# Performance work log

Hardware: AMD Instinct MI355X
Metric: run time of the kernel (lower is better)

Reference implementation:

```python
import jax, jax.numpy as jnp
import numpy as np
from jax import lax

RES = 14
DIM = 384
KEY_DIM = 32
NUM_HEADS = 12
ATTN_RATIO = 4
NH_KD = KEY_DIM * NUM_HEADS            # 384
DH = ATTN_RATIO * KEY_DIM * NUM_HEADS  # 1536
HQKV = DH + 2 * NH_KD                  # 2304
BN_EPS = 1e-5


def _bias_idxs():
    ys, xs = np.meshgrid(np.arange(RES), np.arange(RES), indexing='ij')
    ys = ys.reshape(-1); xs = xs.reshape(-1)
    dy = np.abs(ys[:, None] - ys[None, :])
    dx = np.abs(xs[:, None] - xs[None, :])
    return jnp.asarray(dy * RES + dx, dtype=jnp.int32)  # [196,196], 196 unique offsets


def setup_inputs() -> dict:
    key = jax.random.key(0)
    ks = jax.random.split(key, 16)
    B = 128
    x = jax.random.normal(ks[0], (B, DIM, RES, RES), dtype=jnp.float32)
    # qkv: 1x1 conv DIM->HQKV + BN
    qkv_w = jax.random.normal(ks[1], (HQKV, DIM, 1, 1), dtype=jnp.float32) * 0.05
    qkv_g = jax.random.normal(ks[2], (HQKV,), dtype=jnp.float32) * 0.1 + 1.0
    qkv_b = jax.random.normal(ks[3], (HQKV,), dtype=jnp.float32) * 0.1
    qkv_m = jax.random.normal(ks[4], (HQKV,), dtype=jnp.float32) * 0.1
    qkv_v = jax.random.uniform(ks[5], (HQKV,), dtype=jnp.float32) + 0.5
    # dw: depthwise 3x3 conv on q channels + BN
    dw_w = jax.random.normal(ks[6], (NH_KD, 1, 3, 3), dtype=jnp.float32) * 0.2
    dw_g = jax.random.normal(ks[7], (NH_KD,), dtype=jnp.float32) * 0.1 + 1.0
    dw_b = jax.random.normal(ks[8], (NH_KD,), dtype=jnp.float32) * 0.1
    dw_m = jax.random.normal(ks[9], (NH_KD,), dtype=jnp.float32) * 0.1
    dw_v = jax.random.uniform(ks[10], (NH_KD,), dtype=jnp.float32) + 0.5
    # proj: ReLU -> 1x1 conv DH->DIM + BN
    proj_w = jax.random.normal(ks[11], (DIM, DH, 1, 1), dtype=jnp.float32) * 0.05
    proj_g = jax.random.normal(ks[12], (DIM,), dtype=jnp.float32) * 0.1 + 1.0
    proj_b = jax.random.normal(ks[13], (DIM,), dtype=jnp.float32) * 0.1
    proj_m = jax.random.normal(ks[14], (DIM,), dtype=jnp.float32) * 0.1
    proj_v = jax.random.uniform(ks[15], (DIM,), dtype=jnp.float32) + 0.5
    ab = jax.random.normal(jax.random.fold_in(key, 99), (NUM_HEADS, RES * RES), dtype=jnp.float32) * 0.1
    return {
        'x': x,
        'qkv_w': qkv_w, 'qkv_g': qkv_g, 'qkv_b': qkv_b, 'qkv_m': qkv_m, 'qkv_v': qkv_v,
        'dw_w': dw_w, 'dw_g': dw_g, 'dw_b': dw_b, 'dw_m': dw_m, 'dw_v': dw_v,
        'proj_w': proj_w, 'proj_g': proj_g, 'proj_b': proj_b, 'proj_m': proj_m, 'proj_v': proj_v,
        'attn_biases': ab,
        'bias_idxs': _bias_idxs(),
    }


def _bn(x, g, b, m, v):
    scale = g / jnp.sqrt(v + BN_EPS)
    return x * scale[None, :, None, None] + (b - m * scale)[None, :, None, None]


def reference(x, qkv_w, qkv_g, qkv_b, qkv_m, qkv_v,
              dw_w, dw_g, dw_b, dw_m, dw_v,
              proj_w, proj_g, proj_b, proj_m, proj_v,
              attn_biases, bias_idxs):
    B, _, H, W = x.shape
    n = H * W
    scale = KEY_DIM ** -0.5
    # 1x1 conv + BN
    qkv = jnp.einsum('bchw,oc->bohw', x, qkv_w[:, :, 0, 0])
    qkv = _bn(qkv, qkv_g, qkv_b, qkv_m, qkv_v)
    q = qkv[:, :NH_KD]
    k = qkv[:, NH_KD:2 * NH_KD]
    v = qkv[:, 2 * NH_KD:]
    # depthwise 3x3 conv + BN on q
    q = lax.conv_general_dilated(q, dw_w, (1, 1), ((1, 1), (1, 1)),
                                 dimension_numbers=('NCHW', 'OIHW', 'NCHW'),
                                 feature_group_count=NH_KD)
    q = _bn(q, dw_g, dw_b, dw_m, dw_v)
    # heads: [b, h, d, n]
    q = q.reshape(B, NUM_HEADS, KEY_DIM, n)
    k = k.reshape(B, NUM_HEADS, KEY_DIM, n)
    v = v.reshape(B, NUM_HEADS, ATTN_RATIO * KEY_DIM, n)
    bias = attn_biases[:, bias_idxs]  # [h, n, n]
    attn = jnp.einsum('bhdn,bhdm->bhnm', q, k) * scale + bias[None]
    attn = jax.nn.softmax(attn, axis=-1)
    out = jnp.einsum('bhdm,bhnm->bhdn', v, attn).reshape(B, DH, H, W)
    out = jax.nn.relu(out)
    out = jnp.einsum('bchw,oc->bohw', out, proj_w[:, :, 0, 0])
    return _bn(out, proj_g, proj_b, proj_m, proj_v)
```

## Files before the change

### kernel.cpp

```cpp
#include <hip/hip_runtime.h>

typedef __bf16 bf16;
typedef bf16 bf16x8 __attribute__((ext_vector_type(8)));
typedef bf16 bf16x4 __attribute__((ext_vector_type(4)));
typedef short short4v __attribute__((ext_vector_type(4)));
typedef float f32x4 __attribute__((ext_vector_type(4)));

#define NPIX 196
#define CIN 384
#define NHEADS 12
#define MPAD 224
#define VSTRIDE 232
#define OSTRIDE 40

__device__ __forceinline__ float ldf(const void* p, size_t i, int f) {
    return f ? ((const float*)p)[i] : (float)((const bf16*)p)[i];
}

__device__ __forceinline__ void gld16(const void* g, void* lds_wave_base) {
    __builtin_amdgcn_global_load_lds(
        (const __attribute__((address_space(1))) void*)(unsigned long long)g,
        (__attribute__((address_space(3))) void*)(unsigned long long)lds_wave_base,
        16, 0, 0);
}

__device__ __forceinline__ f32x4 mfma16(bf16x4 a, bf16x4 b, f32x4 c) {
#if __has_builtin(__builtin_amdgcn_mfma_f32_16x16x16bf16_1k)
    return __builtin_amdgcn_mfma_f32_16x16x16bf16_1k(
        __builtin_bit_cast(short4v, a), __builtin_bit_cast(short4v, b), c, 0, 0, 0);
#else
    asm volatile("v_mfma_f32_16x16x16_bf16 %0, %1, %2, %0" : "+v"(c) : "v"(a), "v"(b));
    return c;
#endif
}

__device__ __forceinline__ f32x4 vmax4(f32x4 a, f32x4 b) {
    f32x4 r;
    r[0] = fmaxf(a[0], b[0]);
    r[1] = fmaxf(a[1], b[1]);
    r[2] = fmaxf(a[2], b[2]);
    r[3] = fmaxf(a[3], b[3]);
    return r;
}

__global__ void detect_kernel(const unsigned int* __restrict__ x, int* __restrict__ flag) {
    __shared__ int cnt;
    if (threadIdx.x == 0) cnt = 0;
    __syncthreads();
    int c = 0;
#pragma unroll
    for (int k = 0; k < 8; k++) {
        unsigned int w = x[threadIdx.x * 8 + k];
        unsigned int e = (w >> 7) & 0xFFu;
        if (e > 200u) c++;
    }
    atomicAdd(&cnt, c);
    __syncthreads();
    if (threadIdx.x == 0) *flag = (cnt >= 16) ? 1 : 0;
}

__global__ void convert_kernel(const void* __restrict__ src, bf16* __restrict__ dst, int n,
                               const int* __restrict__ flag) {
    int f = *flag;
    for (int i = blockIdx.x * 256 + threadIdx.x; i < n; i += gridDim.x * 256)
        dst[i] = (bf16)ldf(src, i, f);
}

__global__ void transpose_x_kernel(const void* __restrict__ x, const int* __restrict__ flag,
                                   bf16* __restrict__ xt, int b0) {
    __shared__ bf16 tile[32][33];
    int f = *flag;
    int b = blockIdx.z, gb = b0 + b;
    int c0 = blockIdx.y * 32;
    int hw0 = blockIdx.x * 32;
    int tx = threadIdx.x, ty = threadIdx.y;
    int hw = hw0 + tx, c = c0 + ty;
    if (hw < NPIX) tile[ty][tx] = (bf16)ldf(x, ((size_t)gb * CIN + c) * NPIX + hw, f);
    __syncthreads();
    int hw2 = hw0 + ty, c2 = c0 + tx;
    if (hw2 < NPIX) xt[((size_t)b * NPIX + hw2) * CIN + c2] = tile[tx][ty];
}

__device__ __forceinline__ void gemm_tile(const bf16* __restrict__ A, const bf16* __restrict__ B,
                                          int K, bf16* As, bf16* Bs, f32x4 acc[4][4]) {
    int tid = threadIdx.x;
    int wave = tid >> 6, lane = tid & 63;
    int wm = wave >> 1, wn = wave & 1;
    int row = lane & 15, grp = lane >> 4;
    int sr = lane >> 3;
    int scg = (lane & 7) ^ sr;
    const bf16* Ag = A + (size_t)(wave * 8 + sr) * K + scg * 8;
    const bf16* Bg = B + (size_t)(wave * 8 + sr) * K + scg * 8;
    for (int kb = 0; kb < K; kb += 64) {
        __syncthreads();
#pragma unroll
        for (int p = 0; p < 4; p++) {
            gld16(Ag + (size_t)(p * 32) * K + kb, As + (p * 256 + wave * 64) * 8);
            gld16(Bg + (size_t)(p * 32) * K + kb, Bs + (p * 256 + wave * 64) * 8);
        }
        __syncthreads();
#pragma unroll
        for (int ki = 0; ki < 2; ki++) {
            bf16x8 af[4], bfr[4];
#pragma unroll
            for (int t = 0; t < 4; t++) {
                int ra = wm * 64 + t * 16 + row;
                af[t] = *(const bf16x8*)(As + ra * 64 + (((ki * 4 + grp) ^ (ra & 7)) * 8));
                int rb = wn * 64 + t * 16 + row;
                bfr[t] = *(const bf16x8*)(Bs + rb * 64 + (((ki * 4 + grp) ^ (rb & 7)) * 8));
            }
#pragma unroll
            for (int mt = 0; mt < 4; mt++)
#pragma unroll
                for (int nt = 0; nt < 4; nt++)
                    acc[mt][nt] =
                        __builtin_amdgcn_mfma_f32_16x16x32_bf16(af[mt], bfr[nt], acc[mt][nt], 0, 0, 0);
        }
    }
}

__global__ __launch_bounds__(256) void gemm_qkv_kernel(
    const bf16* __restrict__ xt, const bf16* __restrict__ w,
    const void* __restrict__ g, const void* __restrict__ bb,
    const void* __restrict__ mm, const void* __restrict__ vv, const int* __restrict__ flag,
    bf16* __restrict__ qb, bf16* __restrict__ kt, bf16* __restrict__ vb) {
    __shared__ bf16 As[128 * 64];
    __shared__ bf16 Bs[128 * 64];
    f32x4 acc[4][4];
#pragma unroll
    for (int i = 0; i < 4; i++)
#pragma unroll
        for (int j = 0; j < 4; j++) acc[i][j] = (f32x4){0.f, 0.f, 0.f, 0.f};
    int m0 = blockIdx.x * 128, n0 = blockIdx.y * 128;
    gemm_tile(w + (size_t)m0 * CIN, xt + (size_t)n0 * CIN, CIN, As, Bs, acc);
    int f = *flag;
    int wave = threadIdx.x >> 6, lane = threadIdx.x & 63;
    int wm = wave >> 1, wn = wave & 1, row = lane & 15, grp = lane >> 4;
#pragma unroll
    for (int mt = 0; mt < 4; mt++) {
#pragma unroll
        for (int r = 0; r < 4; r++) {
            int o = m0 + wm * 64 + mt * 16 + grp * 4 + r;
            float scv = ldf(g, o, f) * rsqrtf(ldf(vv, o, f) + 1e-5f);
            float sh = ldf(bb, o, f) - ldf(mm, o, f) * scv;
#pragma unroll
            for (int nt = 0; nt < 4; nt++) {
                int n = n0 + wn * 64 + nt * 16 + row;
                int b = n / NPIX, hw = n - b * NPIX;
                float val = acc[mt][nt][r] * scv + sh;
                bf16 bv = (bf16)val;
                if (o < 384) {
                    qb[((size_t)b * 384 + o) * NPIX + hw] = bv;
                } else if (o < 768) {
                    kt[((size_t)b * NPIX + hw) * CIN + (o - 384)] = bv;
                } else {
                    vb[((size_t)b * 1536 + (o - 768)) * MPAD + hw] = bv;
                }
            }
        }
    }
}

__global__ __launch_bounds__(256) void gemm_proj_kernel(
    const bf16* __restrict__ ot, const bf16* __restrict__ w,
    const void* __restrict__ g, const void* __restrict__ bb,
    const void* __restrict__ mm, const void* __restrict__ vv, const int* __restrict__ flag,
    void* __restrict__ out, int b0) {
    __shared__ bf16 As[128 * 64];
    __shared__ bf16 Bs[128 * 64];
    f32x4 acc[4][4];
#pragma unroll
    for (int i = 0; i < 4; i++)
#pragma unroll
        for (int j = 0; j < 4; j++) acc[i][j] = (f32x4){0.f, 0.f, 0.f, 0.f};
    int m0 = blockIdx.x * 128, n0 = blockIdx.y * 128;
    gemm_tile(w + (size_t)m0 * 1536, ot + (size_t)n0 * 1536, 1536, As, Bs, acc);
    int f = *flag;
    int wave = threadIdx.x >> 6, lane = threadIdx.x & 63;
    int wm = wave >> 1, wn = wave & 1, row = lane & 15, grp = lane >> 4;
#pragma unroll
    for (int mt = 0; mt < 4; mt++) {
#pragma unroll
        for (int r = 0; r < 4; r++) {
            int o = m0 + wm * 64 + mt * 16 + grp * 4 + r;
            float scv = ldf(g, o, f) * rsqrtf(ldf(vv, o, f) + 1e-5f);
            float sh = ldf(bb, o, f) - ldf(mm, o, f) * scv;
#pragma unroll
            for (int nt = 0; nt < 4; nt++) {
                int n = n0 + wn * 64 + nt * 16 + row;
                int b = n / NPIX, hw = n - b * NPIX;
                float val = acc[mt][nt][r] * scv + sh;
                size_t oidx = ((size_t)(b0 + b) * 384 + o) * NPIX + hw;
                if (f) ((float*)out)[oidx] = val;
                else ((bf16*)out)[oidx] = (bf16)val;
            }
        }
    }
}

__global__ void dwconv_kernel(const bf16* __restrict__ qb, const bf16* __restrict__ w,
                              const void* __restrict__ g, const void* __restrict__ bb,
                              const void* __restrict__ mm, const void* __restrict__ vv,
                              const int* __restrict__ flag, bf16* __restrict__ qt) {
    __shared__ bf16 tile[32][33];
    int f = *flag;
    int b = blockIdx.z;
    int c0 = blockIdx.y * 32, hw0 = blockIdx.x * 32;
    int tx = threadIdx.x, ty = threadIdx.y;
    int c = c0 + ty, hw = hw0 + tx;
    if (hw < NPIX) {
        int y = hw / 14, x = hw % 14;
        float acc = 0.f;
        const bf16* wp = w + c * 9;
        const bf16* qp = qb + ((size_t)b * 384 + c) * NPIX;
#pragma unroll
        for (int ky = 0; ky < 3; ky++) {
            int yy = y + ky - 1;
            if (yy < 0 || yy >= 14) continue;
#pragma unroll
            for (int kx = 0; kx < 3; kx++) {
                int xx = x + kx - 1;
                if (xx < 0 || xx >= 14) continue;
                acc += (float)qp[yy * 14 + xx] * (float)wp[ky * 3 + kx];
            }
        }
        float sc = ldf(g, c, f) * rsqrtf(ldf(vv, c, f) + 1e-5f);
        float sh = ldf(bb, c, f) - ldf(mm, c, f) * sc;
        tile[ty][tx] = (bf16)(acc * sc + sh);
    }
    __syncthreads();
    int hw2 = hw0 + ty, c2 = c0 + tx;
    if (hw2 < NPIX) qt[((size_t)b * NPIX + hw2) * CIN + c2] = tile[tx][ty];
}

__global__ void bias_gather_kernel(const void* __restrict__ ab, const int* __restrict__ idx,
                                   const int* __restrict__ flag, float* __restrict__ biasf) {
    int f = *flag;
    int t = blockIdx.x * 256 + threadIdx.x;
    if (t >= NHEADS * NPIX * MPAD) return;
    int h = t / (NPIX * MPAD);
    int rem = t - h * (NPIX * MPAD);
    int n = rem / MPAD, m = rem - n * MPAD;
    biasf[t] = (m < NPIX) ? ldf(ab, h * NPIX + idx[n * NPIX + m], f) : -1e30f;
}

__global__ void zero_vpad_kernel(bf16* __restrict__ vb, int rows) {
    int t = blockIdx.x * 256 + threadIdx.x;
    if (t >= rows * 7) return;
    int r = t / 7, c = t - r * 7;
    *(unsigned long long*)(vb + (size_t)r * MPAD + NPIX + c * 4) = 0ull;
}

__global__ __launch_bounds__(256, 2) void attn_kernel(
    const bf16* __restrict__ qt, const bf16* __restrict__ ktp, const bf16* __restrict__ vb,
    const float* __restrict__ biasf, bf16* __restrict__ ot) {
    __shared__ bf16 Vs[128 * VSTRIDE];
    __shared__ bf16 Osh[4][16 * OSTRIDE];
    int h = blockIdx.x, b = blockIdx.y;
    int tid = threadIdx.x;
    int wave = tid >> 6, lane = tid & 63;
    int row = lane & 15, grp = lane >> 4;
    const float scale = 0.17677669529663687f;
    const f32x4 zf = {0.f, 0.f, 0.f, 0.f};

    {
        const bf16* vsrc = vb + ((size_t)b * 1536 + h * 128) * MPAD;
#pragma unroll
        for (int it = 0; it < 14; it++) {
            int i = it * 256 + tid;
            int r = i / 28, gch = i - r * 28;
            *(bf16x8*)(Vs + r * VSTRIDE + gch * 8) = *(const bf16x8*)(vsrc + (size_t)i * 8);
        }
    }
    __syncthreads();

    const bf16* vls = Vs + row * VSTRIDE + grp * 4;

    for (int nb = wave; nb < 13; nb += 4) {
        int n0 = nb * 16;
        int n = n0 + row;
        int nc = n > 195 ? 195 : n;

        bf16x8 aq = *(const bf16x8*)(qt + ((size_t)b * NPIX + nc) * CIN + h * 32 + grp * 8);

        f32x4 sacc[14];
#pragma unroll
        for (int mt = 0; mt < 14; mt++) {
            int krow = mt * 16 + row;
            if (krow > 195) krow = 195;
            bf16x8 ak = *(const bf16x8*)(ktp + ((size_t)b * NPIX + krow) * CIN + h * 32 + grp * 8);
            sacc[mt] = __builtin_amdgcn_mfma_f32_16x16x32_bf16(ak, aq, zf, 0, 0, 0);
        }

        const float* bp = biasf + ((size_t)h * NPIX + nc) * MPAD + grp * 4;
        f32x4 mxv = {-3.4e38f, -3.4e38f, -3.4e38f, -3.4e38f};
#pragma unroll
        for (int mt = 0; mt < 14; mt++) {
            f32x4 bv = *(const f32x4*)(bp + mt * 16);
            f32x4 s = sacc[mt] * scale + bv;
            sacc[mt] = s;
            mxv = vmax4(mxv, s);
        }
        float mx = fmaxf(fmaxf(mxv[0], mxv[1]), fmaxf(mxv[2], mxv[3]));
        mx = fmaxf(mx, __shfl_xor(mx, 16));
        mx = fmaxf(mx, __shfl_xor(mx, 32));

        f32x4 sumv = zf;
        bf16x4 pf[14];
#pragma unroll
        for (int mt = 0; mt < 14; mt++) {
            f32x4 e;
#pragma unroll
            for (int r = 0; r < 4; r++) e[r] = __expf(sacc[mt][r] - mx);
            sumv += e;
            bf16x4 pb;
#pragma unroll
            for (int r = 0; r < 4; r++) pb[r] = (bf16)e[r];
            pf[mt] = pb;
        }
        float sum = (sumv[0] + sumv[1]) + (sumv[2] + sumv[3]);
        sum += __shfl_xor(sum, 16);
        sum += __shfl_xor(sum, 32);
        float inv = 1.f / sum;

        f32x4 oacc[8];
#pragma unroll
        for (int dt = 0; dt < 8; dt++) oacc[dt] = zf;
#pragma unroll
        for (int mt = 0; mt < 14; mt++) {
            bf16x4 p = pf[mt];
#pragma unroll
            for (int dt = 0; dt < 8; dt++) {
                bf16x4 v4 = *(const bf16x4*)(vls + dt * 16 * VSTRIDE + mt * 16);
                oacc[dt] = mfma16(v4, p, oacc[dt]);
            }
        }

        bf16* osw = Osh[wave];
        int r2 = lane >> 2, c2 = lane & 3;
        int n2 = n0 + r2;
        bf16* op = ot + ((size_t)b * NPIX + n2) * 1536 + h * 128;
#pragma unroll
        for (int dp = 0; dp < 4; dp++) {
#pragma unroll
            for (int u = 0; u < 2; u++) {
                int dt = dp * 2 + u;
                bf16x4 o4;
#pragma unroll
                for (int r = 0; r < 4; r++) {
                    float v = oacc[dt][r] * inv;
                    o4[r] = (bf16)(v > 0.f ? v : 0.f);
                }
                *(bf16x4*)(osw + row * OSTRIDE + u * 16 + grp * 4) = o4;
            }
            asm volatile("s_waitcnt lgkmcnt(0)" ::: "memory");
            if (n2 < NPIX) {
                bf16x8 ov = *(const bf16x8*)(osw + r2 * OSTRIDE + c2 * 8);
                *(bf16x8*)(op + dp * 32 + c2 * 8) = ov;
            }
            asm volatile("s_waitcnt lgkmcnt(0)" ::: "memory");
        }
    }
}

extern "C" void kernel_launch(void* const* d_in, const int* in_sizes, int n_in,
                              void* d_out, int out_size, void* d_ws, size_t ws_size,
                              hipStream_t stream) {
    const void* x      = d_in[0];
    const void* qkv_w  = d_in[1];
    const void* qkv_g  = d_in[2];
    const void* qkv_b  = d_in[3];
    const void* qkv_m  = d_in[4];
    const void* qkv_v  = d_in[5];
    const void* dw_w   = d_in[6];
    const void* dw_g   = d_in[7];
    const void* dw_b   = d_in[8];
    const void* dw_m   = d_in[9];
    const void* dw_v   = d_in[10];
    const void* proj_w = d_in[11];
    const void* proj_g = d_in[12];
    const void* proj_b = d_in[13];
    const void* proj_m = d_in[14];
    const void* proj_v = d_in[15];
    const void* ab     = d_in[16];
    const int*  idx    = (const int*)d_in[17];

    char* ws = (char*)d_ws;
    size_t off = 0;
    auto alloc = [&](size_t bytes) { void* p = ws + off; off += (bytes + 255) & ~(size_t)255; return p; };

    int*   flag = (int*)alloc(4);
    bf16*  wq   = (bf16*)alloc((size_t)2304 * 384 * 2);
    bf16*  wp   = (bf16*)alloc((size_t)384 * 1536 * 2);
    bf16*  wd   = (bf16*)alloc((size_t)384 * 9 * 2);
    float* biasf= (float*)alloc((size_t)NHEADS * NPIX * MPAD * 4);
    size_t fixed = off;

    const size_t s_xt = (size_t)NPIX * CIN;
    const size_t s_qb = (size_t)384 * NPIX;
    const size_t s_kt = (size_t)NPIX * 384;
    const size_t s_vb = (size_t)1536 * MPAD;
    const size_t s_ot = (size_t)NPIX * 1536;
    const size_t per_image = (s_xt + s_qb + s_kt + s_vb + s_ot) * 2;

    int CB = 128;
    while (CB > 32 && fixed + (size_t)CB * per_image > ws_size) CB >>= 1;

    bf16* xt  = (bf16*)alloc((size_t)CB * s_xt * 2);
    bf16* qb  = (bf16*)alloc((size_t)CB * s_qb * 2);
    bf16* ktp = (bf16*)alloc((size_t)CB * s_kt * 2);
    bf16* vb  = (bf16*)alloc((size_t)CB * s_vb * 2);
    bf16* ot  = (bf16*)alloc((size_t)CB * s_ot * 2);
    bf16* qt  = xt;

    detect_kernel<<<dim3(1), dim3(256), 0, stream>>>((const unsigned int*)x, flag);
    convert_kernel<<<dim3(256), dim3(256), 0, stream>>>(qkv_w, wq, 2304 * 384, flag);
    convert_kernel<<<dim3(256), dim3(256), 0, stream>>>(proj_w, wp, 384 * 1536, flag);
    convert_kernel<<<dim3(4), dim3(256), 0, stream>>>(dw_w, wd, 384 * 9, flag);
    int bg = (NHEADS * NPIX * MPAD + 255) / 256;
    bias_gather_kernel<<<dim3(bg), dim3(256), 0, stream>>>(ab, idx, flag, biasf);
    int vrows = CB * 1536;
    zero_vpad_kernel<<<dim3((vrows * 7 + 255) / 256), dim3(256), 0, stream>>>(vb, vrows);

    dim3 tb(32, 32);
    for (int b0 = 0; b0 < 128; b0 += CB) {
        int cb = (128 - b0 < CB) ? (128 - b0) : CB;
        int ntiles = (cb * NPIX) / 128;
        transpose_x_kernel<<<dim3(7, 12, cb), tb, 0, stream>>>(x, flag, xt, b0);
        gemm_qkv_kernel<<<dim3(18, ntiles), dim3(256), 0, stream>>>(xt, wq, qkv_g, qkv_b, qkv_m,
                                                                    qkv_v, flag, qb, ktp, vb);
        dwconv_kernel<<<dim3(7, 12, cb), tb, 0, stream>>>(qb, wd, dw_g, dw_b, dw_m, dw_v, flag, qt);
        attn_kernel<<<dim3(NHEADS, cb), dim3(256), 0, stream>>>(qt, ktp, vb, biasf, ot);
        gemm_proj_kernel<<<dim3(3, ntiles), dim3(256), 0, stream>>>(ot, wp, proj_g, proj_b, proj_m,
                                                                    proj_v, flag, d_out, b0);
    }
}
```

Before: 506.7 us.

## Double-buffer GEMM LDS tiles and add XCD-aware block swizzle

The shared GEMM tile loop now uses two LDS buffers, so the next K-slice loads asynchronously while MFMAs run on the current one, and the per-iteration barriers drop from two to one. In addition, the QKV GEMM, projection GEMM and attention kernels remap block IDs so that consecutive logical tiles land on the same XCD, which is meant to improve L2 reuse of shared weight and activation rows. Doubling LDS to 64KB per GEMM block may reduce occupancy.

```diff
diff --git a/kernel.cpp b/kernel.cpp
--- a/kernel.cpp
+++ b/kernel.cpp
@@ -22,6 +22,12 @@
         (const __attribute__((address_space(1))) void*)(unsigned long long)g,
         (__attribute__((address_space(3))) void*)(unsigned long long)lds_wave_base,
         16, 0, 0);
+}
+
+__device__ __forceinline__ int xcd_swizzle(int orig, int nwg) {
+    int q = nwg >> 3, r = nwg & 7;
+    int xcd = orig & 7, idx = orig >> 3;
+    return (xcd < r ? xcd * (q + 1) : r * (q + 1) + (xcd - r) * q) + idx;
 }
 
 __device__ __forceinline__ f32x4 mfma16(bf16x4 a, bf16x4 b, f32x4 c) {
@@ -89,25 +95,37 @@
     int row = lane & 15, grp = lane >> 4;
     int sr = lane >> 3;
     int scg = (lane & 7) ^ sr;
+    const int BUF = 128 * 64;
     const bf16* Ag = A + (size_t)(wave * 8 + sr) * K + scg * 8;
     const bf16* Bg = B + (size_t)(wave * 8 + sr) * K + scg * 8;
+#pragma unroll
+    for (int p = 0; p < 4; p++) {
+        gld16(Ag + (size_t)(p * 32) * K, As + (p * 256 + wave * 64) * 8);
+        gld16(Bg + (size_t)(p * 32) * K, Bs + (p * 256 + wave * 64) * 8);
+    }
+    __syncthreads();
+    int cur = 0;
     for (int kb = 0; kb < K; kb += 64) {
-        __syncthreads();
-#pragma unroll
-        for (int p = 0; p < 4; p++) {
-            gld16(Ag + (size_t)(p * 32) * K + kb, As + (p * 256 + wave * 64) * 8);
-            gld16(Bg + (size_t)(p * 32) * K + kb, Bs + (p * 256 + wave * 64) * 8);
-        }
-        __syncthreads();
+        if (kb + 64 < K) {
+            bf16* Asn = As + (cur ^ 1) * BUF;
+            bf16* Bsn = Bs + (cur ^ 1) * BUF;
+#pragma unroll
+            for (int p = 0; p < 4; p++) {
+                gld16(Ag + (size_t)(p * 32) * K + kb + 64, Asn + (p * 256 + wave * 64) * 8);
+                gld16(Bg + (size_t)(p * 32) * K + kb + 64, Bsn + (p * 256 + wave * 64) * 8);
+            }
+        }
+        const bf16* Asc = As + cur * BUF;
+        const bf16* Bsc = Bs + cur * BUF;
 #pragma unroll
         for (int ki = 0; ki < 2; ki++) {
             bf16x8 af[4], bfr[4];
 #pragma unroll
             for (int t = 0; t < 4; t++) {
                 int ra = wm * 64 + t * 16 + row;
-                af[t] = *(const bf16x8*)(As + ra * 64 + (((ki * 4 + grp) ^ (ra & 7)) * 8));
+                af[t] = *(const bf16x8*)(Asc + ra * 64 + (((ki * 4 + grp) ^ (ra & 7)) * 8));
                 int rb = wn * 64 + t * 16 + row;
-                bfr[t] = *(const bf16x8*)(Bs + rb * 64 + (((ki * 4 + grp) ^ (rb & 7)) * 8));
+                bfr[t] = *(const bf16x8*)(Bsc + rb * 64 + (((ki * 4 + grp) ^ (rb & 7)) * 8));
             }
 #pragma unroll
             for (int mt = 0; mt < 4; mt++)
@@ -115,6 +133,10 @@
                 for (int nt = 0; nt < 4; nt++)
                     acc[mt][nt] =
                         __builtin_amdgcn_mfma_f32_16x16x32_bf16(af[mt], bfr[nt], acc[mt][nt], 0, 0, 0);
+        }
+        if (kb + 64 < K) {
+            __syncthreads();
+            cur ^= 1;
         }
     }
 }
@@ -124,14 +146,16 @@
     const void* __restrict__ g, const void* __restrict__ bb,
     const void* __restrict__ mm, const void* __restrict__ vv, const int* __restrict__ flag,
     bf16* __restrict__ qb, bf16* __restrict__ kt, bf16* __restrict__ vb) {
-    __shared__ bf16 As[128 * 64];
-    __shared__ bf16 Bs[128 * 64];
+    __shared__ bf16 As[2 * 128 * 64];
+    __shared__ bf16 Bs[2 * 128 * 64];
     f32x4 acc[4][4];
 #pragma unroll
     for (int i = 0; i < 4; i++)
 #pragma unroll
         for (int j = 0; j < 4; j++) acc[i][j] = (f32x4){0.f, 0.f, 0.f, 0.f};
-    int m0 = blockIdx.x * 128, n0 = blockIdx.y * 128;
+    int nwg = gridDim.x * gridDim.y;
+    int l = xcd_swizzle(blockIdx.y * gridDim.x + blockIdx.x, nwg);
+    int m0 = (l % gridDim.x) * 128, n0 = (l / gridDim.x) * 128;
     gemm_tile(w + (size_t)m0 * CIN, xt + (size_t)n0 * CIN, CIN, As, Bs, acc);
     int f = *flag;
     int wave = threadIdx.x >> 6, lane = threadIdx.x & 63;
@@ -166,14 +190,16 @@
     const void* __restrict__ g, const void* __restrict__ bb,
     const void* __restrict__ mm, const void* __restrict__ vv, const int* __restrict__ flag,
     void* __restrict__ out, int b0) {
-    __shared__ bf16 As[128 * 64];
-    __shared__ bf16 Bs[128 * 64];
+    __shared__ bf16 As[2 * 128 * 64];
+    __shared__ bf16 Bs[2 * 128 * 64];
     f32x4 acc[4][4];
 #pragma unroll
     for (int i = 0; i < 4; i++)
 #pragma unroll
         for (int j = 0; j < 4; j++) acc[i][j] = (f32x4){0.f, 0.f, 0.f, 0.f};
-    int m0 = blockIdx.x * 128, n0 = blockIdx.y * 128;
+    int nwg = gridDim.x * gridDim.y;
+    int l = xcd_swizzle(blockIdx.y * gridDim.x + blockIdx.x, nwg);
+    int m0 = (l % gridDim.x) * 128, n0 = (l / gridDim.x) * 128;
     gemm_tile(w + (size_t)m0 * 1536, ot + (size_t)n0 * 1536, 1536, As, Bs, acc);
     int f = *flag;
     int wave = threadIdx.x >> 6, lane = threadIdx.x & 63;
@@ -256,7 +282,9 @@
     const float* __restrict__ biasf, bf16* __restrict__ ot) {
     __shared__ bf16 Vs[128 * VSTRIDE];
     __shared__ bf16 Osh[4][16 * OSTRIDE];
-    int h = blockIdx.x, b = blockIdx.y;
+    int nwg = gridDim.x * gridDim.y;
+    int l = xcd_swizzle(blockIdx.y * gridDim.x + blockIdx.x, nwg);
+    int h = l % NHEADS, b = l / NHEADS;
     int tid = threadIdx.x;
     int wave = tid >> 6, lane = tid & 63;
     int row = lane & 15, grp = lane >> 4;
```

Measured after the change: 488.0 us. -3.7%, faster.
